# Kernel tuning notes

Measured on AMD Instinct MI355X. Metric: run time of the kernel, lower is better.

Reference implementation:

```python
import jax, jax.numpy as jnp
import numpy as np

N, IN_C, HID, OUT_C = 50000, 128, 256, 40
L, G = 4, 2
GC = HID // G  # 128 channels per group
E = 600000
EPS = 1e-5


def _ln(h, g, b):
    mu = jnp.mean(h, axis=-1, keepdims=True)
    var = jnp.mean((h - mu) ** 2, axis=-1, keepdims=True)
    return (h - mu) * jax.lax.rsqrt(var + EPS) * g + b


def setup_inputs() -> dict:
    key = jax.random.key(0)
    ks = jax.random.split(key, 16)
    s = lambda k, shape, sc=0.05: jax.random.normal(k, shape, dtype=jnp.float32) * sc
    return {
        "x": jax.random.normal(ks[0], (N, IN_C), dtype=jnp.float32),
        "edge_index": jax.random.randint(ks[1], (2, E), 0, N, dtype=jnp.int64),
        "edge_weight": jax.random.uniform(ks[2], (E,), dtype=jnp.float32),
        "lin1_w": s(ks[3], (IN_C, HID)),
        "lin1_b": jnp.zeros((HID,), jnp.float32),
        "lin2_w": s(ks[4], (HID, OUT_C)),
        "lin2_b": jnp.zeros((OUT_C,), jnp.float32),
        "norm_g": jnp.ones((L, G, GC), jnp.float32),   # per-block LayerNorm gamma
        "norm_b": jnp.zeros((L, G, GC), jnp.float32),  # per-block LayerNorm beta
        "conv_w": s(ks[5], (L, G, GC, GC)),            # per-block GCNConv weight
        "conv_b": jnp.zeros((L, G, GC), jnp.float32),  # per-block GCNConv bias
        "fnorm_g": jnp.ones((HID,), jnp.float32),
        "fnorm_b": jnp.zeros((HID,), jnp.float32),
    }


def reference(x, edge_index, edge_weight, lin1_w, lin1_b, lin2_w, lin2_b,
              norm_g, norm_b, conv_w, conv_b, fnorm_g, fnorm_b):
    src, dst = edge_index[0], edge_index[1]
    h = x @ lin1_w + lin1_b  # [N, HID]
    for l in range(L):
        xs = jnp.split(h, G, axis=-1)  # G x [N, GC]
        ys = []
        y_in = xs[-1]  # GroupAddRev coupling: y_i = x_i + F_i(y_{i-1}), y_{-1} = x_{G-1}
        for g in range(G):
            # GNNBlock: LayerNorm -> ReLU -> GCNConv(normalize=False)
            z = jax.nn.relu(_ln(y_in, norm_g[l, g], norm_b[l, g]))
            z = z @ conv_w[l, g]                       # GCNConv linear
            msg = edge_weight[:, None] * z[src]        # [E, GC]
            agg = jax.ops.segment_sum(msg, dst, num_segments=N) + conv_b[l, g]
            y_in = xs[g] + agg
            ys.append(y_in)
        h = jnp.concatenate(ys, axis=-1)
    h = jax.nn.relu(_ln(h, fnorm_g, fnorm_b))
    return h @ lin2_w + lin2_b  # [N, OUT_C]
```

## Files before the change

### kernel.cpp

```cpp
#include <hip/hip_runtime.h>
#include <stdint.h>

#define NN    50000
#define INC   128
#define HIDC  256
#define OUTC  40
#define GCH   128
#define NL    4
#define NG    2
#define NEDGE 600000
#define EPSV  1e-5f

typedef __bf16 bf16x8 __attribute__((ext_vector_type(8)));
typedef float  f32x4  __attribute__((ext_vector_type(4)));
typedef unsigned short u16x4 __attribute__((ext_vector_type(4)));
typedef unsigned short u16x8 __attribute__((ext_vector_type(8)));

__device__ __forceinline__ float bf2f(unsigned short u) {
    union { float f; unsigned int i; } v;
    v.i = ((unsigned int)u) << 16;
    return v.f;
}
__device__ __forceinline__ unsigned short f2bf(float f) {
    union { float f; unsigned int i; } v;
    v.f = f;
    unsigned int u = v.i;
    u += 0x7FFFu + ((u >> 16) & 1u);
    return (unsigned short)(u >> 16);
}
__device__ __forceinline__ float ldf(const void* p, int is_f32, long long i) {
    if (is_f32) return ((const float*)p)[i];
    return bf2f(((const unsigned short*)p)[i]);
}
__device__ __forceinline__ bf16x8 ld8(const unsigned short* p) {
    return *(const bf16x8*)p;
}
__device__ __forceinline__ void gload_lds16(const void* g, void* l) {
    __builtin_amdgcn_global_load_lds(
        (const __attribute__((address_space(1))) unsigned int*)g,
        (__attribute__((address_space(3))) unsigned int*)l,
        16, 0, 0);
}

__global__ void k_marker(void* out, float val, int n) {
    int i = blockIdx.x * 256 + threadIdx.x;
    if (i < n) ((unsigned short*)out)[i] = f2bf(val);
}

#define CVT_W1  32768
#define CVT_CW  131072
#define CVT_W2  12288
#define CVT_TOT (CVT_W1 + CVT_CW + CVT_W2)

__global__ void k_prep(const void* x, const int* ei,
                       const void* w1, const void* cw, const void* w2,
                       const void* b1, const void* ng, const void* nb, const void* cb,
                       const void* fg, const void* fb, const void* b2,
                       int* flags, int* deg,
                       unsigned short* w1t, unsigned short* cwt, unsigned short* w2t,
                       float* b1f, float* ngf, float* nbf, float* cbf,
                       float* fgf, float* fbf, float* b2f) {
    int t = threadIdx.x, b = blockIdx.x;
    if (b < 196) {
        int gid = b * 256 + t;
        if (gid < NN) deg[gid] = 0;
        if (b == 0) {
            __shared__ int hi_or, wild_cnt;
            if (t == 0) { hi_or = 0; wild_cnt = 0; }
            __syncthreads();
            int acc = 0;
            for (int i = 0; i < 8; i++) acc |= ei[2 * (t + i * 256) + 1];
            if (acc) atomicOr(&hi_or, 1);
            int wild = 0;
            for (int i = 0; i < 2; i++) {
                unsigned short u = ((const unsigned short*)x)[t + i * 256];
                int e = (u >> 7) & 0xFF;
                if (e <= 0x30 || e >= 0xC0) wild++;
            }
            atomicAdd(&wild_cnt, wild);
            __syncthreads();
            if (t == 0) {
                flags[0] = hi_or ? 0 : 1;
                flags[1] = (wild_cnt > 32) ? 1 : 0;
            }
        }
        return;
    }
    __shared__ int wc;
    if (t == 0) wc = 0;
    __syncthreads();
    int wild = 0;
    for (int i = 0; i < 2; i++) {
        unsigned short u = ((const unsigned short*)x)[t + i * 256];
        int e = (u >> 7) & 0xFF;
        if (e <= 0x30 || e >= 0xC0) wild++;
    }
    atomicAdd(&wc, wild);
    __syncthreads();
    int f32 = (wc > 32) ? 1 : 0;
    int cb2 = b - 196;
    if (cb2 == 688) {
        b1f[t] = ldf(b1, f32, t);
        fgf[t] = ldf(fg, f32, t);
        fbf[t] = ldf(fb, f32, t);
        if (t < 48) b2f[t] = (t < OUTC) ? ldf(b2, f32, t) : 0.0f;
        for (int i = 0; i < 4; i++) {
            int j = t + i * 256;
            ngf[j] = ldf(ng, f32, j);
            nbf[j] = ldf(nb, f32, j);
            cbf[j] = ldf(cb, f32, j);
        }
        return;
    }
    long long j = (long long)cb2 * 256 + t;
    if (j >= CVT_TOT) return;
    if (j < CVT_W1) {
        int n = (int)(j >> 7), k = (int)(j & 127);
        w1t[n * 128 + (k ^ ((n & 7) << 3))] = f2bf(ldf(w1, f32, (long long)k * HIDC + n));
    } else if (j < CVT_W1 + CVT_CW) {
        long long jj = j - CVT_W1;
        int lg = (int)(jj >> 14);
        int rem = (int)(jj & 16383);
        int n = rem >> 7, k = rem & 127;
        cwt[lg * 16384 + n * 128 + (k ^ ((n & 7) << 3))] =
            f2bf(ldf(cw, f32, (long long)lg * GCH * GCH + (long long)k * GCH + n));
    } else {
        long long jj = j - (CVT_W1 + CVT_CW);
        int n = (int)(jj >> 8), k = (int)(jj & 255);
        w2t[n * 256 + (k ^ ((n & 7) << 3))] =
            (n < OUTC) ? f2bf(ldf(w2, f32, (long long)k * OUTC + n)) : (unsigned short)0;
    }
}

__global__ void k_count(const int* __restrict__ ei, const int* __restrict__ flags,
                        int* __restrict__ deg) {
    int e = (blockIdx.x * 256 + threadIdx.x) * 2;
    if (e >= NEDGE) return;
    int d0, d1;
    if (flags[0]) {
        int4 v = *(const int4*)(ei + 2 * (NEDGE + e));
        d0 = v.x; d1 = v.z;
    } else {
        int2 v = *(const int2*)(ei + NEDGE + e);
        d0 = v.x; d1 = v.y;
    }
    atomicAdd(&deg[d0], 1);
    if (e + 1 < NEDGE) atomicAdd(&deg[d1], 1);
}

#define SCAN_B 49
__global__ void k_scan(const int* __restrict__ deg,
                       int* __restrict__ rowptr, int* __restrict__ cursor) {
    __shared__ int part[256];
    __shared__ int bbase_s;
    int b = blockIdx.x, t = threadIdx.x;
    int lim = b * 1024;
    int pre = 0;
    for (int i = t; i < lim; i += 256) pre += deg[i];
    part[t] = pre;
    __syncthreads();
    for (int off = 128; off > 0; off >>= 1) {
        if (t < off) part[t] += part[t + off];
        __syncthreads();
    }
    if (t == 0) bbase_s = part[0];
    __syncthreads();

    int base = b * 1024 + t * 4;
    int v[4];
    int s = 0;
#pragma unroll
    for (int j = 0; j < 4; j++) {
        int i = base + j;
        v[j] = (i < NN) ? deg[i] : 0;
        s += v[j];
    }
    part[t] = s;
    __syncthreads();
    for (int off = 1; off < 256; off <<= 1) {
        int x = (t >= off) ? part[t - off] : 0;
        __syncthreads();
        part[t] += x;
        __syncthreads();
    }
    int run = bbase_s + part[t] - s;
#pragma unroll
    for (int j = 0; j < 4; j++) {
        int i = base + j;
        if (i < NN) { rowptr[i] = run; cursor[i] = run; }
        run += v[j];
    }
    if (b == SCAN_B - 1 && t == 255) rowptr[NN] = NEDGE;
}

#define FIRST_B 782
__global__ __launch_bounds__(256, 5) void k_firstfill(
    const void* __restrict__ x,
    const unsigned short* __restrict__ w1t,
    const float* __restrict__ b1f,
    const float* __restrict__ ngf, const float* __restrict__ nbf,
    const unsigned short* __restrict__ cw0,
    const int* __restrict__ flags,
    unsigned short* __restrict__ h,
    unsigned short* __restrict__ z0,
    const int* __restrict__ ei, const void* __restrict__ ew,
    int* __restrict__ cursor, unsigned int* __restrict__ epk)
{
    __shared__ __align__(16) unsigned short xb[64 * 128];
    __shared__ __align__(16) unsigned short wt[64 * 128];
    int t = threadIdx.x;
    int f32x = flags[1];

    if (blockIdx.x >= FIRST_B) {
        int e = ((blockIdx.x - FIRST_B) * 256 + t) * 2;
        if (e >= NEDGE) return;
        int is64 = flags[0];
        int d0, s0, d1 = 0, s1 = 0;
        int has1 = (e + 1 < NEDGE);
        if (is64) {
            d0 = ei[2 * (NEDGE + e)];
            s0 = ei[2 * e];
            if (has1) { d1 = ei[2 * (NEDGE + e) + 2]; s1 = ei[2 * e + 2]; }
        } else {
            d0 = ei[NEDGE + e];
            s0 = ei[e];
            if (has1) { d1 = ei[NEDGE + e + 1]; s1 = ei[e + 1]; }
        }
        int p0 = atomicAdd(&cursor[d0], 1);
        int p1 = has1 ? atomicAdd(&cursor[d1], 1) : 0;
        unsigned int w0 = f2bf(ldf(ew, f32x, e));
        epk[p0] = (w0 << 16) | (unsigned int)s0;
        if (has1) {
            unsigned int w1v = f2bf(ldf(ew, f32x, e + 1));
            epk[p1] = (w1v << 16) | (unsigned int)s1;
        }
        return;
    }

    int r0 = blockIdx.x * 64;
    int w = t >> 6, lane = t & 63, quad = lane >> 4, ln = lane & 15;
    const f32x4 zf = {0.f, 0.f, 0.f, 0.f};

#pragma unroll
    for (int i = 0; i < 4; i++) {
        int cb = (i * 256 + t) * 16;
        gload_lds16((const char*)w1t + cb, (char*)wt + cb);
    }
#pragma unroll
    for (int i = 0; i < 4; i++) {
        int chunk = i * 256 + t;
        int row = chunk >> 4, c16 = chunk & 15;
        int grow = r0 + row;
        u16x8 val = {0, 0, 0, 0, 0, 0, 0, 0};
        if (grow < NN) {
            if (f32x) {
                const float* p = (const float*)x + (long long)grow * INC + c16 * 8;
                float4 a = *(const float4*)p;
                float4 c = *(const float4*)(p + 4);
                val[0] = f2bf(a.x); val[1] = f2bf(a.y); val[2] = f2bf(a.z); val[3] = f2bf(a.w);
                val[4] = f2bf(c.x); val[5] = f2bf(c.y); val[6] = f2bf(c.z); val[7] = f2bf(c.w);
            } else {
                val = *(const u16x8*)((const unsigned short*)x + (long long)grow * INC + c16 * 8);
            }
        }
        *(u16x8*)((char*)xb + row * 256 + ((c16 * 16) ^ ((row & 7) << 4))) = val;
    }
    __syncthreads();

    f32x4 acc[2][8];
#pragma unroll
    for (int i = 0; i < 2; i++)
#pragma unroll
        for (int j = 0; j < 8; j++) acc[i][j] = zf;

#pragma unroll
    for (int ph = 0; ph < 4; ph++) {
        int nh = ph >> 1, s = ph & 1;
#pragma unroll
        for (int kk = 0; kk < 4; kk++) {
            int cb = kk * 64 + quad * 16;
            int rA = w * 16 + ln;
            bf16x8 a = *(const bf16x8*)((const char*)xb + rA * 256 + (cb ^ ((rA & 7) << 4)));
#pragma unroll
            for (int nfl = 0; nfl < 4; nfl++) {
                int rB = nfl * 16 + ln;
                bf16x8 b = *(const bf16x8*)((const char*)wt + rB * 256 + (cb ^ ((rB & 7) << 4)));
                acc[nh][s * 4 + nfl] =
                    __builtin_amdgcn_mfma_f32_16x16x32_bf16(a, b, acc[nh][s * 4 + nfl], 0, 0, 0);
            }
        }
        __syncthreads();
        if (ph < 3) {
#pragma unroll
            for (int i = 0; i < 4; i++) {
                int cb = (i * 256 + t) * 16;
                gload_lds16((const char*)w1t + (ph + 1) * 16384 + cb, (char*)wt + cb);
            }
            __syncthreads();
        }
    }

#pragma unroll
    for (int i = 0; i < 4; i++) {
        int cb = (i * 256 + t) * 16;
        gload_lds16((const char*)cw0 + cb, (char*)wt + cb);
    }

    float ga8[8], be8[8], yv[8][4];
#pragma unroll
    for (int nf = 0; nf < 8; nf++) {
        int col = nf * 16 + ln;
        float b0 = b1f[col], b1 = b1f[128 + col];
        ga8[nf] = ngf[col]; be8[nf] = nbf[col];
#pragma unroll
        for (int r4 = 0; r4 < 4; r4++) {
            int row = r0 + w * 16 + quad * 4 + r4;
            unsigned short h0 = f2bf(acc[0][nf][r4] + b0);
            unsigned short h1 = f2bf(acc[1][nf][r4] + b1);
            if (row < NN) {
                h[(long long)row * HIDC + col] = h0;
                h[(long long)row * HIDC + 128 + col] = h1;
            }
            yv[nf][r4] = bf2f(h1);
        }
    }
    unsigned short* a_tile = xb;
#pragma unroll
    for (int r4 = 0; r4 < 4; r4++) {
        float s = 0.f, q = 0.f;
#pragma unroll
        for (int nf = 0; nf < 8; nf++) { s += yv[nf][r4]; q += yv[nf][r4] * yv[nf][r4]; }
        s += __shfl_xor(s, 1, 64); s += __shfl_xor(s, 2, 64);
        s += __shfl_xor(s, 4, 64); s += __shfl_xor(s, 8, 64);
        q += __shfl_xor(q, 1, 64); q += __shfl_xor(q, 2, 64);
        q += __shfl_xor(q, 4, 64); q += __shfl_xor(q, 8, 64);
        float mu = s * (1.0f / GCH);
        float var = q * (1.0f / GCH) - mu * mu;
        float rs = rsqrtf(var + EPSV);
        int row = w * 16 + quad * 4 + r4;
#pragma unroll
        for (int nf = 0; nf < 8; nf++) {
            float val = (yv[nf][r4] - mu) * rs * ga8[nf] + be8[nf];
            if (val < 0.f) val = 0.f;
            *(unsigned short*)((char*)a_tile + row * 256 +
                               (((nf * 16 + ln) * 2) ^ ((row & 7) << 4))) = f2bf(val);
        }
    }
    __syncthreads();

    f32x4 acc2[8];
#pragma unroll
    for (int j = 0; j < 8; j++) acc2[j] = zf;
#pragma unroll
    for (int s = 0; s < 2; s++) {
#pragma unroll
        for (int kk = 0; kk < 4; kk++) {
            int cb = kk * 64 + quad * 16;
            int rA = w * 16 + ln;
            bf16x8 a = *(const bf16x8*)((const char*)a_tile + rA * 256 + (cb ^ ((rA & 7) << 4)));
#pragma unroll
            for (int nfl = 0; nfl < 4; nfl++) {
                int rB = nfl * 16 + ln;
                bf16x8 b = *(const bf16x8*)((const char*)wt + rB * 256 + (cb ^ ((rB & 7) << 4)));
                acc2[s * 4 + nfl] =
                    __builtin_amdgcn_mfma_f32_16x16x32_bf16(a, b, acc2[s * 4 + nfl], 0, 0, 0);
            }
        }
        if (s == 0) {
            __syncthreads();
#pragma unroll
            for (int i = 0; i < 4; i++) {
                int cb = (i * 256 + t) * 16;
                gload_lds16((const char*)cw0 + 16384 + cb, (char*)wt + cb);
            }
            __syncthreads();
        }
    }
#pragma unroll
    for (int nf = 0; nf < 8; nf++) {
        int col = nf * 16 + ln;
#pragma unroll
        for (int r4 = 0; r4 < 4; r4++) {
            int row2 = r0 + w * 16 + quad * 4 + r4;
            if (row2 < NN) z0[(long long)row2 * GCH + col] = f2bf(acc2[nf][r4]);
        }
    }
}

__global__ __launch_bounds__(256, 5) void k_fused(
    const int* __restrict__ rowptr, const unsigned int* __restrict__ epk,
    const unsigned short* __restrict__ zin,
    const float* __restrict__ cb,
    unsigned short* __restrict__ h, int out_half,
    const float* __restrict__ ga, const float* __restrict__ be,
    const unsigned short* __restrict__ cwn,
    unsigned short* __restrict__ zout)
{
    __shared__ __align__(16) unsigned short wt[64 * 128];
    __shared__ __align__(16) unsigned short a_tile[64 * 128];
    int t = threadIdx.x;
    int r0 = blockIdx.x * 64;
    int c8 = (t & 15) << 3;

#pragma unroll
    for (int i = 0; i < 4; i++) {
        int cbyte = (i * 256 + t) * 16;
        gload_lds16((const char*)cwn + cbyte, (char*)wt + cbyte);
    }

    int begA[4], endA[4];
#pragma unroll
    for (int bt = 0; bt < 4; bt++) {
        int node = r0 + bt * 16 + (t >> 4);
        begA[bt] = (node < NN) ? rowptr[node] : 0;
        endA[bt] = (node < NN) ? rowptr[node + 1] : 0;
    }

#pragma unroll 1
    for (int bt = 0; bt < 4; bt++) {
        int row = bt * 16 + (t >> 4);
        int node = r0 + row;
        if (node < NN) {
            int beg = begA[bt], end = endA[bt];
            unsigned short* hp = h + (long long)node * HIDC + out_half * GCH + c8;
            u16x8 hv = *(u16x8*)hp;
            const unsigned short* zb = zin + c8;
            float acc[8];
#pragma unroll
            for (int j = 0; j < 8; j++) acc[j] = 0.f;

            int e = beg;
            for (; e + 7 < end; e += 8) {
                unsigned int pe[8];
                u16x8 v[8];
#pragma unroll
                for (int i = 0; i < 8; i++) pe[i] = epk[e + i];
#pragma unroll
                for (int i = 0; i < 8; i++)
                    v[i] = *(const u16x8*)(zb + (long long)(pe[i] & 0xFFFFu) * GCH);
#pragma unroll
                for (int i = 0; i < 8; i++) {
                    float wv = bf2f((unsigned short)(pe[i] >> 16));
#pragma unroll
                    for (int j = 0; j < 8; j++) acc[j] += wv * bf2f(v[i][j]);
                }
            }
            if (e + 3 < end) {
                unsigned int pe[4];
                u16x8 v[4];
#pragma unroll
                for (int i = 0; i < 4; i++) pe[i] = epk[e + i];
#pragma unroll
                for (int i = 0; i < 4; i++)
                    v[i] = *(const u16x8*)(zb + (long long)(pe[i] & 0xFFFFu) * GCH);
#pragma unroll
                for (int i = 0; i < 4; i++) {
                    float wv = bf2f((unsigned short)(pe[i] >> 16));
#pragma unroll
                    for (int j = 0; j < 8; j++) acc[j] += wv * bf2f(v[i][j]);
                }
                e += 4;
            }
            for (; e < end; e++) {
                unsigned int pe = epk[e];
                float w0 = bf2f((unsigned short)(pe >> 16));
                u16x8 v = *(const u16x8*)(zb + (long long)(pe & 0xFFFFu) * GCH);
#pragma unroll
                for (int j = 0; j < 8; j++) acc[j] += w0 * bf2f(v[j]);
            }

            float y[8]; float sum = 0.f, sq = 0.f;
#pragma unroll
            for (int j = 0; j < 8; j++) {
                float yy = bf2f(hv[j]) + acc[j] + cb[c8 + j];
                unsigned short r = f2bf(yy);
                hv[j] = r;
                y[j] = bf2f(r);
                sum += y[j]; sq += y[j] * y[j];
            }
            *(u16x8*)hp = hv;

            sum += __shfl_xor(sum, 1, 64); sum += __shfl_xor(sum, 2, 64);
            sum += __shfl_xor(sum, 4, 64); sum += __shfl_xor(sum, 8, 64);
            sq  += __shfl_xor(sq, 1, 64);  sq  += __shfl_xor(sq, 2, 64);
            sq  += __shfl_xor(sq, 4, 64);  sq  += __shfl_xor(sq, 8, 64);
            float mu = sum * (1.0f / GCH);
            float var = sq * (1.0f / GCH) - mu * mu;
            float rs = rsqrtf(var + EPSV);
            u16x8 o;
#pragma unroll
            for (int j = 0; j < 8; j++) {
                float val = (y[j] - mu) * rs * ga[c8 + j] + be[c8 + j];
                if (val < 0.f) val = 0.f;
                o[j] = f2bf(val);
            }
            *(u16x8*)((char*)a_tile + row * 256 + ((c8 * 2) ^ ((row & 7) << 4))) = o;
        }
    }
    __syncthreads();

    int w = t >> 6, lane = t & 63, quad = lane >> 4, ln = lane & 15;
    const f32x4 zf = {0.f, 0.f, 0.f, 0.f};
    f32x4 acc2[8];
#pragma unroll
    for (int j = 0; j < 8; j++) acc2[j] = zf;
#pragma unroll
    for (int s = 0; s < 2; s++) {
#pragma unroll
        for (int kk = 0; kk < 4; kk++) {
            int cbyte = kk * 64 + quad * 16;
            int rA = w * 16 + ln;
            bf16x8 a = *(const bf16x8*)((const char*)a_tile + rA * 256 + (cbyte ^ ((rA & 7) << 4)));
#pragma unroll
            for (int nfl = 0; nfl < 4; nfl++) {
                int rB = nfl * 16 + ln;
                bf16x8 b = *(const bf16x8*)((const char*)wt + rB * 256 + (cbyte ^ ((rB & 7) << 4)));
                acc2[s * 4 + nfl] =
                    __builtin_amdgcn_mfma_f32_16x16x32_bf16(a, b, acc2[s * 4 + nfl], 0, 0, 0);
            }
        }
        if (s == 0) {
            __syncthreads();
#pragma unroll
            for (int i = 0; i < 4; i++) {
                int cbyte = (i * 256 + t) * 16;
                gload_lds16((const char*)cwn + 16384 + cbyte, (char*)wt + cbyte);
            }
            __syncthreads();
        }
    }
#pragma unroll
    for (int nf = 0; nf < 8; nf++) {
        int col = nf * 16 + ln;
#pragma unroll
        for (int r4 = 0; r4 < 4; r4++) {
            int row2 = r0 + w * 16 + quad * 4 + r4;
            if (row2 < NN) zout[(long long)row2 * GCH + col] = f2bf(acc2[nf][r4]);
        }
    }
}

__global__ __launch_bounds__(256, 5) void k_last(
    const int* __restrict__ rowptr, const unsigned int* __restrict__ epk,
    const unsigned short* __restrict__ zin,
    const float* __restrict__ cb,
    unsigned short* __restrict__ h,
    const float* __restrict__ fgf, const float* __restrict__ fbf,
    const unsigned short* __restrict__ w2t,
    const float* __restrict__ b2f,
    const int* __restrict__ flags,
    void* __restrict__ out)
{
    __shared__ __align__(16) unsigned short a_tile[64 * 256];
    int t = threadIdx.x;
    int r0 = blockIdx.x * 64;
    int c8 = (t & 15) << 3;
    const int out_half = 1;

    int begA[4], endA[4];
#pragma unroll
    for (int bt = 0; bt < 4; bt++) {
        int node = r0 + bt * 16 + (t >> 4);
        begA[bt] = (node < NN) ? rowptr[node] : 0;
        endA[bt] = (node < NN) ? rowptr[node + 1] : 0;
    }

#pragma unroll 1
    for (int bt = 0; bt < 4; bt++) {
        int row = bt * 16 + (t >> 4);
        int node = r0 + row;
        if (node < NN) {
            int beg = begA[bt], end = endA[bt];
            unsigned short* hp = h + (long long)node * HIDC + out_half * GCH + c8;
            u16x8 hv = *(u16x8*)hp;
            const unsigned short* zb = zin + c8;
            float acc[8];
#pragma unroll
            for (int j = 0; j < 8; j++) acc[j] = 0.f;

            int e = beg;
            for (; e + 7 < end; e += 8) {
                unsigned int pe[8];
                u16x8 v[8];
#pragma unroll
                for (int i = 0; i < 8; i++) pe[i] = epk[e + i];
#pragma unroll
                for (int i = 0; i < 8; i++)
                    v[i] = *(const u16x8*)(zb + (long long)(pe[i] & 0xFFFFu) * GCH);
#pragma unroll
                for (int i = 0; i < 8; i++) {
                    float wv = bf2f((unsigned short)(pe[i] >> 16));
#pragma unroll
                    for (int j = 0; j < 8; j++) acc[j] += wv * bf2f(v[i][j]);
                }
            }
            if (e + 3 < end) {
                unsigned int pe[4];
                u16x8 v[4];
#pragma unroll
                for (int i = 0; i < 4; i++) pe[i] = epk[e + i];
#pragma unroll
                for (int i = 0; i < 4; i++)
                    v[i] = *(const u16x8*)(zb + (long long)(pe[i] & 0xFFFFu) * GCH);
#pragma unroll
                for (int i = 0; i < 4; i++) {
                    float wv = bf2f((unsigned short)(pe[i] >> 16));
#pragma unroll
                    for (int j = 0; j < 8; j++) acc[j] += wv * bf2f(v[i][j]);
                }
                e += 4;
            }
            for (; e < end; e++) {
                unsigned int pe = epk[e];
                float w0 = bf2f((unsigned short)(pe >> 16));
                u16x8 v = *(const u16x8*)(zb + (long long)(pe & 0xFFFFu) * GCH);
#pragma unroll
                for (int j = 0; j < 8; j++) acc[j] += w0 * bf2f(v[j]);
            }

            float y[8]; float sum = 0.f, sq = 0.f;
#pragma unroll
            for (int j = 0; j < 8; j++) {
                float yy = bf2f(hv[j]) + acc[j] + cb[c8 + j];
                unsigned short r = f2bf(yy);
                hv[j] = r;
                y[j] = bf2f(r);
                sum += y[j]; sq += y[j] * y[j];
            }
            *(u16x8*)hp = hv;

            float oy[8];
            u16x8 ov = *(const u16x8*)(h + (long long)node * HIDC + (out_half ^ 1) * GCH + c8);
#pragma unroll
            for (int j = 0; j < 8; j++) {
                oy[j] = bf2f(ov[j]);
                sum += oy[j]; sq += oy[j] * oy[j];
            }
            sum += __shfl_xor(sum, 1, 64); sum += __shfl_xor(sum, 2, 64);
            sum += __shfl_xor(sum, 4, 64); sum += __shfl_xor(sum, 8, 64);
            sq  += __shfl_xor(sq, 1, 64);  sq  += __shfl_xor(sq, 2, 64);
            sq  += __shfl_xor(sq, 4, 64);  sq  += __shfl_xor(sq, 8, 64);
            float mu = sum * (1.0f / HIDC);
            float var = sq * (1.0f / HIDC) - mu * mu;
            float rs = rsqrtf(var + EPSV);

            u16x8 o;
            int cn = out_half * GCH + c8;
#pragma unroll
            for (int j = 0; j < 8; j++) {
                float val = (y[j] - mu) * rs * fgf[cn + j] + fbf[cn + j];
                if (val < 0.f) val = 0.f;
                o[j] = f2bf(val);
            }
            *(u16x8*)((char*)a_tile + row * 512 + ((cn * 2) ^ ((row & 7) << 4))) = o;
            int co = (out_half ^ 1) * GCH + c8;
#pragma unroll
            for (int j = 0; j < 8; j++) {
                float val = (oy[j] - mu) * rs * fgf[co + j] + fbf[co + j];
                if (val < 0.f) val = 0.f;
                o[j] = f2bf(val);
            }
            *(u16x8*)((char*)a_tile + row * 512 + ((co * 2) ^ ((row & 7) << 4))) = o;
        }
    }
    __syncthreads();

    int w = t >> 6, lane = t & 63, quad = lane >> 4, ln = lane & 15;
    const f32x4 zf = {0.f, 0.f, 0.f, 0.f};
    f32x4 acc2[3];
#pragma unroll
    for (int j = 0; j < 3; j++) acc2[j] = zf;
#pragma unroll
    for (int kk = 0; kk < 8; kk++) {
        int cbyte = kk * 64 + quad * 16;
        int ko = kk * 32 + quad * 8;
        int row = w * 16 + ln;
        bf16x8 a = *(const bf16x8*)((const char*)a_tile + row * 512 + (cbyte ^ ((row & 7) << 4)));
#pragma unroll
        for (int nf = 0; nf < 3; nf++) {
            int rB = nf * 16 + ln;
            bf16x8 b = ld8(w2t + rB * 256 + (ko ^ ((rB & 7) << 3)));
            acc2[nf] = __builtin_amdgcn_mfma_f32_16x16x32_bf16(a, b, acc2[nf], 0, 0, 0);
        }
    }
    int f32o = flags[1];
#pragma unroll
    for (int nf = 0; nf < 3; nf++) {
        int col = nf * 16 + ln;
        if (col >= OUTC) continue;
        float bias = b2f[col];
#pragma unroll
        for (int r4 = 0; r4 < 4; r4++) {
            int row2 = r0 + w * 16 + quad * 4 + r4;
            if (row2 < NN) {
                float val = acc2[nf][r4] + bias;
                long long o = (long long)row2 * OUTC + col;
                if (f32o) ((float*)out)[o] = val;
                else      ((unsigned short*)out)[o] = f2bf(val);
            }
        }
    }
}

extern "C" void kernel_launch(void* const* d_in, const int* in_sizes, int n_in,
                              void* d_out, int out_size, void* d_ws, size_t ws_size,
                              hipStream_t stream)
{
    const void* x       = d_in[0];
    const int*  ei      = (const int*)d_in[1];
    const void* ew      = d_in[2];
    const void* lin1_w  = d_in[3];
    const void* lin1_b  = d_in[4];
    const void* lin2_w  = d_in[5];
    const void* lin2_b  = d_in[6];
    const void* norm_g  = d_in[7];
    const void* norm_b  = d_in[8];
    const void* conv_w  = d_in[9];
    const void* conv_b  = d_in[10];
    const void* fnorm_g = d_in[11];
    const void* fnorm_b = d_in[12];

    char* ws = (char*)d_ws;
    size_t off = 0;
    auto alloc = [&](size_t bytes) { void* p = (void*)(ws + off); off += (bytes + 255) & ~255ull; return p; };

    unsigned short* h      = (unsigned short*)alloc((size_t)NN * HIDC * 2);
    unsigned short* z0     = (unsigned short*)alloc((size_t)NN * GCH * 2);
    unsigned short* z1     = (unsigned short*)alloc((size_t)NN * GCH * 2);
    unsigned short* w1t    = (unsigned short*)alloc((size_t)CVT_W1 * 2);
    unsigned short* cwt    = (unsigned short*)alloc((size_t)CVT_CW * 2);
    unsigned short* w2t    = (unsigned short*)alloc((size_t)CVT_W2 * 2);
    float*          b1f    = (float*)alloc(256 * 4);
    float*          ngf    = (float*)alloc(1024 * 4);
    float*          nbf    = (float*)alloc(1024 * 4);
    float*          cbf    = (float*)alloc(1024 * 4);
    float*          fgf    = (float*)alloc(256 * 4);
    float*          fbf    = (float*)alloc(256 * 4);
    float*          b2f    = (float*)alloc(48 * 4);
    int*            deg    = (int*)alloc((size_t)NN * 4);
    int*            rowptr = (int*)alloc(((size_t)NN + 1) * 4);
    int*            cursor = (int*)alloc((size_t)NN * 4);
    unsigned int*   epk    = (unsigned int*)alloc((size_t)NEDGE * 4);
    int*            flags  = (int*)alloc(256);

    if (ws_size < off || n_in < 13) {
        float mv = 100.0f + (float)(ws_size >> 20) + ((n_in < 13) ? 10000.0f : 0.0f);
        k_marker<<<(out_size + 255) / 256, 256, 0, stream>>>(d_out, mv, out_size);
        return;
    }

    k_prep<<<885, 256, 0, stream>>>(x, ei, lin1_w, conv_w, lin2_w,
                                    lin1_b, norm_g, norm_b, conv_b,
                                    fnorm_g, fnorm_b, lin2_b,
                                    flags, deg, w1t, cwt, w2t,
                                    b1f, ngf, nbf, cbf, fgf, fbf, b2f);
    k_count<<<(NEDGE / 2 + 255) / 256, 256, 0, stream>>>(ei, flags, deg);
    k_scan<<<SCAN_B, 256, 0, stream>>>(deg, rowptr, cursor);

    const int FILL_B = (NEDGE / 2 + 255) / 256;
    k_firstfill<<<FIRST_B + FILL_B, 256, 0, stream>>>(x, w1t, b1f, ngf, nbf, cwt,
                                                      flags, h, z0,
                                                      ei, ew, cursor, epk);
    for (int lg = 0; lg < NL * NG - 1; lg++) {
        unsigned short* zin  = (lg & 1) ? z1 : z0;
        unsigned short* zout = (lg & 1) ? z0 : z1;
        k_fused<<<FIRST_B, 256, 0, stream>>>(rowptr, epk, zin, cbf + lg * GCH, h, lg & 1,
                                             ngf + (lg + 1) * GCH, nbf + (lg + 1) * GCH,
                                             cwt + (size_t)(lg + 1) * 16384, zout);
    }
    k_last<<<FIRST_B, 256, 0, stream>>>(rowptr, epk, z1, cbf + 7 * GCH, h,
                                        fgf, fbf, w2t, b2f, flags, d_out);
}
```

Baseline: 497.4 us.

## Use 512-thread blocks for fused aggregation and split edge fill into own kernel

The fused gather/LayerNorm/GEMM kernels now run 512 threads per 64-row tile. Each thread handles two rows instead of four, which doubles the gather parallelism per block. The whole 128x128 conv weight is loaded into LDS at once, so the mid-kernel syncs and reload are gone, and the eight waves split the output columns into two halves. The CSR fill is moved out of the combined first kernel into its own launch, which adds a launch and removes its overlap with the first GEMM. LDS per block rises, which may limit occupancy, and in the last kernel half the waves sit idle during the final GEMM.

```diff
diff --git a/kernel.cpp b/kernel.cpp
--- a/kernel.cpp
+++ b/kernel.cpp
@@ -193,8 +193,35 @@
     if (b == SCAN_B - 1 && t == 255) rowptr[NN] = NEDGE;
 }
 
-#define FIRST_B 782
-__global__ __launch_bounds__(256, 5) void k_firstfill(
+__global__ void k_fill(const int* __restrict__ ei, const void* __restrict__ ew,
+                       const int* __restrict__ flags,
+                       int* __restrict__ cursor, unsigned int* __restrict__ epk) {
+    int e = (blockIdx.x * 256 + threadIdx.x) * 2;
+    if (e >= NEDGE) return;
+    int is64 = flags[0];
+    int f32 = flags[1];
+    int d0, s0, d1 = 0, s1 = 0;
+    int has1 = (e + 1 < NEDGE);
+    if (is64) {
+        d0 = ei[2 * (NEDGE + e)];
+        s0 = ei[2 * e];
+        if (has1) { d1 = ei[2 * (NEDGE + e) + 2]; s1 = ei[2 * e + 2]; }
+    } else {
+        d0 = ei[NEDGE + e];
+        s0 = ei[e];
+        if (has1) { d1 = ei[NEDGE + e + 1]; s1 = ei[e + 1]; }
+    }
+    int p0 = atomicAdd(&cursor[d0], 1);
+    int p1 = has1 ? atomicAdd(&cursor[d1], 1) : 0;
+    unsigned int w0 = f2bf(ldf(ew, f32, e));
+    epk[p0] = (w0 << 16) | (unsigned int)s0;
+    if (has1) {
+        unsigned int w1 = f2bf(ldf(ew, f32, e + 1));
+        epk[p1] = (w1 << 16) | (unsigned int)s1;
+    }
+}
+
+__global__ __launch_bounds__(256, 5) void k_first(
     const void* __restrict__ x,
     const unsigned short* __restrict__ w1t,
     const float* __restrict__ b1f,
@@ -202,42 +229,13 @@
     const unsigned short* __restrict__ cw0,
     const int* __restrict__ flags,
     unsigned short* __restrict__ h,
-    unsigned short* __restrict__ z0,
-    const int* __restrict__ ei, const void* __restrict__ ew,
-    int* __restrict__ cursor, unsigned int* __restrict__ epk)
+    unsigned short* __restrict__ z0)
 {
     __shared__ __align__(16) unsigned short xb[64 * 128];
     __shared__ __align__(16) unsigned short wt[64 * 128];
     int t = threadIdx.x;
+    int r0 = blockIdx.x * 64;
     int f32x = flags[1];
-
-    if (blockIdx.x >= FIRST_B) {
-        int e = ((blockIdx.x - FIRST_B) * 256 + t) * 2;
-        if (e >= NEDGE) return;
-        int is64 = flags[0];
-        int d0, s0, d1 = 0, s1 = 0;
-        int has1 = (e + 1 < NEDGE);
-        if (is64) {
-            d0 = ei[2 * (NEDGE + e)];
-            s0 = ei[2 * e];
-            if (has1) { d1 = ei[2 * (NEDGE + e) + 2]; s1 = ei[2 * e + 2]; }
-        } else {
-            d0 = ei[NEDGE + e];
-            s0 = ei[e];
-            if (has1) { d1 = ei[NEDGE + e + 1]; s1 = ei[e + 1]; }
-        }
-        int p0 = atomicAdd(&cursor[d0], 1);
-        int p1 = has1 ? atomicAdd(&cursor[d1], 1) : 0;
-        unsigned int w0 = f2bf(ldf(ew, f32x, e));
-        epk[p0] = (w0 << 16) | (unsigned int)s0;
-        if (has1) {
-            unsigned int w1v = f2bf(ldf(ew, f32x, e + 1));
-            epk[p1] = (w1v << 16) | (unsigned int)s1;
-        }
-        return;
-    }
-
-    int r0 = blockIdx.x * 64;
     int w = t >> 6, lane = t & 63, quad = lane >> 4, ln = lane & 15;
     const f32x4 zf = {0.f, 0.f, 0.f, 0.f};
 
@@ -387,7 +385,7 @@
     }
 }
 
-__global__ __launch_bounds__(256, 5) void k_fused(
+__global__ __launch_bounds__(512, 6) void k_fused(
     const int* __restrict__ rowptr, const unsigned int* __restrict__ epk,
     const unsigned short* __restrict__ zin,
     const float* __restrict__ cb,
@@ -396,7 +394,7 @@
     const unsigned short* __restrict__ cwn,
     unsigned short* __restrict__ zout)
 {
-    __shared__ __align__(16) unsigned short wt[64 * 128];
+    __shared__ __align__(16) unsigned short wt[128 * 128];
     __shared__ __align__(16) unsigned short a_tile[64 * 128];
     int t = threadIdx.x;
     int r0 = blockIdx.x * 64;
@@ -404,21 +402,21 @@
 
 #pragma unroll
     for (int i = 0; i < 4; i++) {
-        int cbyte = (i * 256 + t) * 16;
+        int cbyte = (i * 512 + t) * 16;
         gload_lds16((const char*)cwn + cbyte, (char*)wt + cbyte);
     }
 
-    int begA[4], endA[4];
-#pragma unroll
-    for (int bt = 0; bt < 4; bt++) {
-        int node = r0 + bt * 16 + (t >> 4);
+    int begA[2], endA[2];
+#pragma unroll
+    for (int bt = 0; bt < 2; bt++) {
+        int node = r0 + bt * 32 + (t >> 4);
         begA[bt] = (node < NN) ? rowptr[node] : 0;
         endA[bt] = (node < NN) ? rowptr[node + 1] : 0;
     }
 
 #pragma unroll 1
-    for (int bt = 0; bt < 4; bt++) {
-        int row = bt * 16 + (t >> 4);
+    for (int bt = 0; bt < 2; bt++) {
+        int row = bt * 32 + (t >> 4);
         int node = r0 + row;
         if (node < NN) {
             int beg = begA[bt], end = endA[bt];
@@ -500,47 +498,35 @@
     __syncthreads();
 
     int w = t >> 6, lane = t & 63, quad = lane >> 4, ln = lane & 15;
+    int wr = w & 3, ch = w >> 2;
     const f32x4 zf = {0.f, 0.f, 0.f, 0.f};
-    f32x4 acc2[8];
-#pragma unroll
-    for (int j = 0; j < 8; j++) acc2[j] = zf;
-#pragma unroll
-    for (int s = 0; s < 2; s++) {
-#pragma unroll
-        for (int kk = 0; kk < 4; kk++) {
-            int cbyte = kk * 64 + quad * 16;
-            int rA = w * 16 + ln;
-            bf16x8 a = *(const bf16x8*)((const char*)a_tile + rA * 256 + (cbyte ^ ((rA & 7) << 4)));
-#pragma unroll
-            for (int nfl = 0; nfl < 4; nfl++) {
-                int rB = nfl * 16 + ln;
-                bf16x8 b = *(const bf16x8*)((const char*)wt + rB * 256 + (cbyte ^ ((rB & 7) << 4)));
-                acc2[s * 4 + nfl] =
-                    __builtin_amdgcn_mfma_f32_16x16x32_bf16(a, b, acc2[s * 4 + nfl], 0, 0, 0);
-            }
-        }
-        if (s == 0) {
-            __syncthreads();
-#pragma unroll
-            for (int i = 0; i < 4; i++) {
-                int cbyte = (i * 256 + t) * 16;
-                gload_lds16((const char*)cwn + 16384 + cbyte, (char*)wt + cbyte);
-            }
-            __syncthreads();
-        }
-    }
-#pragma unroll
-    for (int nf = 0; nf < 8; nf++) {
-        int col = nf * 16 + ln;
+    f32x4 acc2[4];
+#pragma unroll
+    for (int j = 0; j < 4; j++) acc2[j] = zf;
+#pragma unroll
+    for (int kk = 0; kk < 4; kk++) {
+        int cbyte = kk * 64 + quad * 16;
+        int rA = wr * 16 + ln;
+        bf16x8 a = *(const bf16x8*)((const char*)a_tile + rA * 256 + (cbyte ^ ((rA & 7) << 4)));
+#pragma unroll
+        for (int nfl = 0; nfl < 4; nfl++) {
+            int rB = ch * 64 + nfl * 16 + ln;
+            bf16x8 b = *(const bf16x8*)((const char*)wt + rB * 256 + (cbyte ^ ((rB & 7) << 4)));
+            acc2[nfl] = __builtin_amdgcn_mfma_f32_16x16x32_bf16(a, b, acc2[nfl], 0, 0, 0);
+        }
+    }
+#pragma unroll
+    for (int nfl = 0; nfl < 4; nfl++) {
+        int col = ch * 64 + nfl * 16 + ln;
 #pragma unroll
         for (int r4 = 0; r4 < 4; r4++) {
-            int row2 = r0 + w * 16 + quad * 4 + r4;
-            if (row2 < NN) zout[(long long)row2 * GCH + col] = f2bf(acc2[nf][r4]);
-        }
-    }
-}
-
-__global__ __launch_bounds__(256, 5) void k_last(
+            int row2 = r0 + wr * 16 + quad * 4 + r4;
+            if (row2 < NN) zout[(long long)row2 * GCH + col] = f2bf(acc2[nfl][r4]);
+        }
+    }
+}
+
+__global__ __launch_bounds__(512, 6) void k_last(
     const int* __restrict__ rowptr, const unsigned int* __restrict__ epk,
     const unsigned short* __restrict__ zin,
     const float* __restrict__ cb,
@@ -557,17 +543,17 @@
     int c8 = (t & 15) << 3;
     const int out_half = 1;
 
-    int begA[4], endA[4];
-#pragma unroll
-    for (int bt = 0; bt < 4; bt++) {
-        int node = r0 + bt * 16 + (t >> 4);
+    int begA[2], endA[2];
+#pragma unroll
+    for (int bt = 0; bt < 2; bt++) {
+        int node = r0 + bt * 32 + (t >> 4);
         begA[bt] = (node < NN) ? rowptr[node] : 0;
         endA[bt] = (node < NN) ? rowptr[node + 1] : 0;
     }
 
 #pragma unroll 1
-    for (int bt = 0; bt < 4; bt++) {
-        int row = bt * 16 + (t >> 4);
+    for (int bt = 0; bt < 2; bt++) {
+        int row = bt * 32 + (t >> 4);
         int node = r0 + row;
         if (node < NN) {
             int beg = begA[bt], end = endA[bt];
@@ -666,37 +652,39 @@
     __syncthreads();
 
     int w = t >> 6, lane = t & 63, quad = lane >> 4, ln = lane & 15;
-    const f32x4 zf = {0.f, 0.f, 0.f, 0.f};
-    f32x4 acc2[3];
-#pragma unroll
-    for (int j = 0; j < 3; j++) acc2[j] = zf;
-#pragma unroll
-    for (int kk = 0; kk < 8; kk++) {
-        int cbyte = kk * 64 + quad * 16;
-        int ko = kk * 32 + quad * 8;
-        int row = w * 16 + ln;
-        bf16x8 a = *(const bf16x8*)((const char*)a_tile + row * 512 + (cbyte ^ ((row & 7) << 4)));
+    if (w < 4) {
+        const f32x4 zf = {0.f, 0.f, 0.f, 0.f};
+        f32x4 acc2[3];
+#pragma unroll
+        for (int j = 0; j < 3; j++) acc2[j] = zf;
+#pragma unroll
+        for (int kk = 0; kk < 8; kk++) {
+            int cbyte = kk * 64 + quad * 16;
+            int ko = kk * 32 + quad * 8;
+            int row = w * 16 + ln;
+            bf16x8 a = *(const bf16x8*)((const char*)a_tile + row * 512 + (cbyte ^ ((row & 7) << 4)));
+#pragma unroll
+            for (int nf = 0; nf < 3; nf++) {
+                int rB = nf * 16 + ln;
+                bf16x8 b = ld8(w2t + rB * 256 + (ko ^ ((rB & 7) << 3)));
+                acc2[nf] = __builtin_amdgcn_mfma_f32_16x16x32_bf16(a, b, acc2[nf], 0, 0, 0);
+            }
+        }
+        int f32o = flags[1];
 #pragma unroll
         for (int nf = 0; nf < 3; nf++) {
-            int rB = nf * 16 + ln;
-            bf16x8 b = ld8(w2t + rB * 256 + (ko ^ ((rB & 7) << 3)));
-            acc2[nf] = __builtin_amdgcn_mfma_f32_16x16x32_bf16(a, b, acc2[nf], 0, 0, 0);
-        }
-    }
-    int f32o = flags[1];
-#pragma unroll
-    for (int nf = 0; nf < 3; nf++) {
-        int col = nf * 16 + ln;
-        if (col >= OUTC) continue;
-        float bias = b2f[col];
-#pragma unroll
-        for (int r4 = 0; r4 < 4; r4++) {
-            int row2 = r0 + w * 16 + quad * 4 + r4;
-            if (row2 < NN) {
-                float val = acc2[nf][r4] + bias;
-                long long o = (long long)row2 * OUTC + col;
-                if (f32o) ((float*)out)[o] = val;
-                else      ((unsigned short*)out)[o] = f2bf(val);
+            int col = nf * 16 + ln;
+            if (col >= OUTC) continue;
+            float bias = b2f[col];
+#pragma unroll
+            for (int r4 = 0; r4 < 4; r4++) {
+                int row2 = r0 + w * 16 + quad * 4 + r4;
+                if (row2 < NN) {
+                    float val = acc2[nf][r4] + bias;
+                    long long o = (long long)row2 * OUTC + col;
+                    if (f32o) ((float*)out)[o] = val;
+                    else      ((unsigned short*)out)[o] = f2bf(val);
+                }
             }
         }
     }
@@ -756,18 +744,17 @@
                                     b1f, ngf, nbf, cbf, fgf, fbf, b2f);
     k_count<<<(NEDGE / 2 + 255) / 256, 256, 0, stream>>>(ei, flags, deg);
     k_scan<<<SCAN_B, 256, 0, stream>>>(deg, rowptr, cursor);
-
-    const int FILL_B = (NEDGE / 2 + 255) / 256;
-    k_firstfill<<<FIRST_B + FILL_B, 256, 0, stream>>>(x, w1t, b1f, ngf, nbf, cwt,
-                                                      flags, h, z0,
-                                                      ei, ew, cursor, epk);
+    k_fill<<<(NEDGE / 2 + 255) / 256, 256, 0, stream>>>(ei, ew, flags, cursor, epk);
+
+    const int GB = (NN + 63) / 64;
+    k_first<<<GB, 256, 0, stream>>>(x, w1t, b1f, ngf, nbf, cwt, flags, h, z0);
     for (int lg = 0; lg < NL * NG - 1; lg++) {
         unsigned short* zin  = (lg & 1) ? z1 : z0;
         unsigned short* zout = (lg & 1) ? z0 : z1;
-        k_fused<<<FIRST_B, 256, 0, stream>>>(rowptr, epk, zin, cbf + lg * GCH, h, lg & 1,
-                                             ngf + (lg + 1) * GCH, nbf + (lg + 1) * GCH,
-                                             cwt + (size_t)(lg + 1) * 16384, zout);
-    }
-    k_last<<<FIRST_B, 256, 0, stream>>>(rowptr, epk, z1, cbf + 7 * GCH, h,
-                                        fgf, fbf, w2t, b2f, flags, d_out);
-}
+        k_fused<<<GB, 512, 0, stream>>>(rowptr, epk, zin, cbf + lg * GCH, h, lg & 1,
+                                        ngf + (lg + 1) * GCH, nbf + (lg + 1) * GCH,
+                                        cwt + (size_t)(lg + 1) * 16384, zout);
+    }
+    k_last<<<GB, 512, 0, stream>>>(rowptr, epk, z1, cbf + 7 * GCH, h,
+                                   fgf, fbf, w2t, b2f, flags, d_out);
+}
```

Result: slower. 596.9 us (+20.0%).
